# Optimization experiments

Measured on AMD Instinct MI355X. Metric: run time of the kernel, lower is better.

Reference implementation:

```python
import jax, jax.numpy as jnp
import numpy as np

LN_EPS = 1e-6


def setup_inputs() -> dict:
    key = jax.random.key(0)
    ks = jax.random.split(key, 10)
    B, S, D, M, P = 64, 512, 1024, 512, 3
    seq_out = jax.random.normal(ks[0], (B, S, D), dtype=jnp.float32)
    # dependency-tree style adjacency: sparse 0/1, stored dense as in the module
    adj = (jax.random.uniform(ks[1], (B, S, S)) < 0.02).astype(jnp.float32)
    aspect_mask = jax.random.randint(ks[2], (B, S), 0, 2, dtype=jnp.int32)
    # guarantee at least one aspect token per row (asp_wn divisor)
    aspect_mask = aspect_mask.at[:, 0].set(1)
    sc = 0.02
    return {
        "seq_out": seq_out,
        "adj": adj,
        "aspect_mask": aspect_mask,
        "ln_a": jnp.ones((D,), jnp.float32),
        "ln_b": jnp.zeros((D,), jnp.float32),
        "asp_w": jax.random.normal(ks[3], (D,), jnp.float32) * sc,
        "asp_b": jnp.zeros((), jnp.float32),
        "W0": jax.random.normal(ks[4], (D, M), jnp.float32) * sc,
        "b0": jnp.zeros((M,), jnp.float32),
        "W1": jax.random.normal(ks[5], (M, M), jnp.float32) * sc,
        "b1": jnp.zeros((M,), jnp.float32),
        "W2": jax.random.normal(ks[6], (M, M), jnp.float32) * sc,
        "b2": jnp.zeros((M,), jnp.float32),
        "cls_w": jax.random.normal(ks[7], (2 * M, P), jnp.float32) * sc,
        "cls_b": jnp.zeros((P,), jnp.float32),
    }


def _torch_layernorm(x, a, b):
    # torch code: a*(x-mean)/(std+eps)+b with unbiased std (Bessel, /(D-1))
    D = x.shape[-1]
    mean = jnp.mean(x, axis=-1, keepdims=True)
    xc = x - mean
    std = jnp.sqrt(jnp.sum(xc * xc, axis=-1, keepdims=True) / (D - 1))
    return a * xc / (std + LN_EPS) + b


def reference(seq_out, adj, aspect_mask, ln_a, ln_b, asp_w, asp_b,
              W0, b0, W1, b1, W2, b2, cls_w, cls_b):
    tgt = aspect_mask.astype(seq_out.dtype)                 # [B,S] labels == BCE weight (eval mode)
    x = _torch_layernorm(seq_out, ln_a, ln_b)               # [B,S,D]

    # aspect classification head + weighted BCEWithLogits (mean over all elems)
    z = jnp.einsum('bsd,d->bs', x, asp_w) + asp_b           # logits [B,S]
    bce = jnp.logaddexp(0.0, z) - z * tgt                   # stable BCE-with-logits
    loss_asp = jnp.mean(tgt * bce)
    aspect_pred = jax.nn.sigmoid(z)

    # dense-adjacency GCN (dropout = identity in eval)
    denom = jnp.sum(adj, axis=2, keepdims=True) + 1.0       # [B,S,1]
    out = x
    for W, b in ((W0, b0), (W1, b1), (W2, b2)):
        Ax = jnp.einsum('bst,btd->bsd', adj, out)           # aggregate
        out = jax.nn.relu((Ax @ W + b) / denom)             # project + degree-norm + relu

    # aspect-masked mean pool + global mean pool
    asp_wn = jnp.sum(tgt, axis=1, keepdims=True)            # [B,1]
    dep = jnp.einsum('bsm,bs->bm', out, tgt) / asp_wn       # [B,M]
    glob = jnp.mean(out, axis=1)                            # [B,M]

    feature = jnp.concatenate([dep, glob], axis=-1) @ cls_w + cls_b
    logits = jax.nn.softmax(feature, axis=1)
    return feature, logits, aspect_pred, loss_asp
```

## Files before the change

### kernel.cpp

```cpp
#include <hip/hip_runtime.h>
#include <math.h>

typedef __bf16 bf16;
typedef bf16 bf16x2 __attribute__((ext_vector_type(2)));
typedef bf16 bf16x4 __attribute__((ext_vector_type(4)));
typedef bf16 bf16x8 __attribute__((ext_vector_type(8)));
typedef float f32x4 __attribute__((ext_vector_type(4)));

#define NROWS 32768
#define DDIM 1024
#define MDIM 512

__device__ __forceinline__ float wave_reduce_sum(float v) {
#pragma unroll
  for (int o = 32; o > 0; o >>= 1) v += __shfl_down(v, o, 64);
  return v;
}
__device__ __forceinline__ float wave_allreduce_sum(float v) {
#pragma unroll
  for (int o = 32; o > 0; o >>= 1) v += __shfl_xor(v, o, 64);
  return v;
}

__device__ __forceinline__ void load_lds16(const bf16* g, bf16* l) {
  __builtin_amdgcn_global_load_lds(
      (const __attribute__((address_space(1))) unsigned int*)g,
      (__attribute__((address_space(3))) unsigned int*)l, 16, 0, 0);
}

__global__ __launch_bounds__(256) void prep_kernel(
    const float* __restrict__ seq, const float* __restrict__ adj,
    const int* __restrict__ amask, const float* __restrict__ ga,
    const float* __restrict__ gb, const float* __restrict__ aw,
    const float* __restrict__ ab, const float* __restrict__ W0,
    const float* __restrict__ W1, const float* __restrict__ W2,
    bf16* __restrict__ xn, float* __restrict__ aspect_pred,
    float* __restrict__ loss_arr, unsigned short* __restrict__ nbr,
    int* __restrict__ cnt, float* __restrict__ denomv,
    bf16* __restrict__ W0T, bf16* __restrict__ W1T, bf16* __restrict__ W2T) {
  const int bid = blockIdx.x;
  const int tid = threadIdx.x;
  const int lane = tid & 63;
  const int wv = tid >> 6;

  if (bid < 8192) {
    const int row = bid * 4 + wv;
    const float* xr = seq + (size_t)row * DDIM;
    f32x4 v[4];
    float s = 0.0f, sq = 0.0f;
#pragma unroll
    for (int j = 0; j < 4; ++j) {
      v[j] = __builtin_nontemporal_load((const f32x4*)&xr[j * 256 + lane * 4]);
      s += v[j].x + v[j].y + v[j].z + v[j].w;
      sq += v[j].x * v[j].x + v[j].y * v[j].y + v[j].z * v[j].z + v[j].w * v[j].w;
    }
    s = wave_allreduce_sum(s);
    sq = wave_allreduce_sum(sq);
    float mean = s * (1.0f / 1024.0f);
    float var = (sq - 1024.0f * mean * mean) * (1.0f / 1023.0f);
    var = fmaxf(var, 0.0f);
    float inv = 1.0f / (sqrtf(var) + 1e-6f);
    float zp = 0.0f;
#pragma unroll
    for (int j = 0; j < 4; ++j) {
      int c = j * 256 + lane * 4;
      float4 a4 = *(const float4*)&ga[c];
      float4 b4 = *(const float4*)&gb[c];
      float4 w4 = *(const float4*)&aw[c];
      float x0 = a4.x * (v[j].x - mean) * inv + b4.x;
      float x1 = a4.y * (v[j].y - mean) * inv + b4.y;
      float x2 = a4.z * (v[j].z - mean) * inv + b4.z;
      float x3 = a4.w * (v[j].w - mean) * inv + b4.w;
      bf16x4 o;
      o[0] = (bf16)x0; o[1] = (bf16)x1; o[2] = (bf16)x2; o[3] = (bf16)x3;
      __builtin_nontemporal_store(o, (bf16x4*)&xn[(size_t)row * DDIM + c]);
      zp += x0 * w4.x + x1 * w4.y + x2 * w4.z + x3 * w4.w;
    }
    zp = wave_reduce_sum(zp);
    if (lane == 0) {
      float z = zp + ab[0];
      aspect_pred[row] = 1.0f / (1.0f + expf(-z));
      float tgt = (float)amask[row];
      float bce = fmaxf(z, 0.0f) + log1pf(expf(-fabsf(z))) - z * tgt;
      loss_arr[row] = tgt * bce;
    }
  } else if (bid < 16384) {
    const int row = (bid - 8192) * 4 + wv;
    const float* ar = adj + (size_t)row * 512;
    unsigned short* nr = nbr + (size_t)row * 512;
    unsigned long long below = (1ull << lane) - 1ull;
    int base = 0;
#pragma unroll
    for (int t = 0; t < 2; ++t) {
      f32x4 v = __builtin_nontemporal_load((const f32x4*)&ar[t * 256 + lane * 4]);
      unsigned long long m0 = __ballot(v.x != 0.0f);
      unsigned long long m1 = __ballot(v.y != 0.0f);
      unsigned long long m2 = __ballot(v.z != 0.0f);
      unsigned long long m3 = __ballot(v.w != 0.0f);
      int c0 = __popcll(m0), c1 = __popcll(m1), c2 = __popcll(m2);
      int col = t * 256 + lane * 4;
      if (v.x != 0.0f) nr[base + __popcll(m0 & below)] = (unsigned short)(col + 0);
      if (v.y != 0.0f) nr[base + c0 + __popcll(m1 & below)] = (unsigned short)(col + 1);
      if (v.z != 0.0f) nr[base + c0 + c1 + __popcll(m2 & below)] = (unsigned short)(col + 2);
      if (v.w != 0.0f) nr[base + c0 + c1 + c2 + __popcll(m3 & below)] = (unsigned short)(col + 3);
      base += c0 + c1 + c2 + __popcll(m3);
    }
    if (lane == 0) { cnt[row] = base; denomv[row] = (float)base + 1.0f; }
  } else {
    __shared__ bf16 tld[64][72];
    int wid = bid - 16384;
    const float* Wsrc; bf16* Wdst; int KK, NN, t0;
    if (wid < 128)      { Wsrc = W0; Wdst = W0T; KK = 1024; NN = 512; t0 = wid; }
    else if (wid < 192) { Wsrc = W1; Wdst = W1T; KK = 512;  NN = 512; t0 = wid - 128; }
    else                { Wsrc = W2; Wdst = W2T; KK = 512;  NN = 512; t0 = wid - 192; }
    int k0 = (t0 >> 3) << 6;
    int n0 = (t0 & 7) << 6;
    int kk = tid >> 4, nn = (tid & 15) << 2;
#pragma unroll
    for (int s = 0; s < 4; ++s) {
      float4 v = *(const float4*)&Wsrc[(size_t)(k0 + s * 16 + kk) * NN + n0 + nn];
      tld[nn + 0][s * 16 + kk] = (bf16)v.x;
      tld[nn + 1][s * 16 + kk] = (bf16)v.y;
      tld[nn + 2][s * 16 + kk] = (bf16)v.z;
      tld[nn + 3][s * 16 + kk] = (bf16)v.w;
    }
    __syncthreads();
#pragma unroll
    for (int p2 = 0; p2 < 2; ++p2) {
      int seg = p2 * 256 + tid;
      int nn2 = seg >> 3, kk2 = (seg & 7) << 3;
      bf16x8 val;
#pragma unroll
      for (int j = 0; j < 8; ++j) val[j] = tld[nn2][kk2 + j];
      *(bf16x8*)&Wdst[(size_t)(n0 + nn2) * KK + k0 + kk2] = val;
    }
  }
}

#define BAR  __builtin_amdgcn_s_barrier()
#define WAITL do { asm volatile("s_waitcnt lgkmcnt(0)" ::: "memory"); \
                   __builtin_amdgcn_sched_barrier(0); } while (0)
#define WAITV4 do { asm volatile("s_waitcnt vmcnt(4)" ::: "memory"); \
                    __builtin_amdgcn_sched_barrier(0); } while (0)

__global__ __launch_bounds__(512, 2) void gemm256(const bf16* __restrict__ A,
                                                  const bf16* __restrict__ BT,
                                                  bf16* __restrict__ C,
                                                  int K) {
  __shared__ __align__(16) bf16 SMEM[65536];
  bf16 (*As)[16384] = (bf16(*)[16384])SMEM;
  bf16 (*Bs)[16384] = (bf16(*)[16384])(SMEM + 32768);
  const int tid = threadIdx.x;
  const int lane = tid & 63;
  const int wave = tid >> 6;
  const int wr = wave >> 2;
  const int wc = wave & 3;
  const int T = K >> 6;

  const int p = blockIdx.x;
  const int chunk = gridDim.x >> 3;
  const int wg = (p & 7) * chunk + (p >> 3);
  const int m0 = (wg >> 1) * 256;
  const int n0 = (wg & 1) * 256;

  const int srow = tid >> 3;
  const int scol8 = (tid & 7) ^ (srow & 7);

#define STAGEA(t, h)                                                          \
  do {                                                                        \
    int kt_ = ((t) < T) ? (t) * 64 : 0;                                       \
    const bf16* s_ = A + (size_t)(m0 + (h) * 128 + srow) * K + kt_ + scol8*8; \
    bf16* d_ = &As[(t) & 1][(h) * 8192 + wave * 512];                         \
    load_lds16(s_, d_);                                                       \
    load_lds16(s_ + (size_t)64 * K, d_ + 4096);                               \
  } while (0)
#define STAGEB(t, h)                                                          \
  do {                                                                        \
    int kt_ = ((t) < T) ? (t) * 64 : 0;                                       \
    const bf16* s_ = BT + (size_t)(n0 + (h) * 128 + srow) * K + kt_ + scol8*8;\
    bf16* d_ = &Bs[(t) & 1][(h) * 8192 + wave * 512];                         \
    load_lds16(s_, d_);                                                       \
    load_lds16(s_ + (size_t)64 * K, d_ + 4096);                               \
  } while (0)

  const int abase = (wr * 128 + (lane & 15)) * 64 + (lane >> 4) * 8;
  const int bbase = (wc * 64 + (lane & 15)) * 64 + (lane >> 4) * 8;
  const int axor = (lane & 7) << 3;

  bf16x8 areg[4][2], breg[4][2];
  f32x4 acc[8][4];
#pragma unroll
  for (int i = 0; i < 8; ++i)
#pragma unroll
    for (int j = 0; j < 4; ++j)
#pragma unroll
      for (int r = 0; r < 4; ++r) acc[i][j][r] = 0.0f;

#define LDA(buf_, qm)                                                         \
  _Pragma("unroll") for (int i_ = 0; i_ < 4; ++i_)                            \
  _Pragma("unroll") for (int h2_ = 0; h2_ < 2; ++h2_)                         \
    areg[i_][h2_] = *(const bf16x8*)&As[buf_][                                \
        (abase + ((qm)*4 + i_) * 1024 + h2_ * 32) ^ axor];
#define LDB(buf_, qn)                                                         \
  _Pragma("unroll") for (int j_ = 0; j_ < 2; ++j_)                            \
  _Pragma("unroll") for (int h2_ = 0; h2_ < 2; ++h2_)                         \
    breg[(qn)*2 + j_][h2_] = *(const bf16x8*)&Bs[buf_][                       \
        (bbase + ((qn)*2 + j_) * 1024 + h2_ * 32) ^ axor];
#define MFMAQ(qm, qn)                                                         \
  __builtin_amdgcn_s_setprio(1);                                              \
  _Pragma("unroll") for (int i_ = 0; i_ < 4; ++i_)                            \
  _Pragma("unroll") for (int j_ = 0; j_ < 2; ++j_)                            \
  _Pragma("unroll") for (int h2_ = 0; h2_ < 2; ++h2_)                         \
    acc[(qm)*4 + i_][(qn)*2 + j_] = __builtin_amdgcn_mfma_f32_16x16x32_bf16(  \
        areg[i_][h2_], breg[(qn)*2 + j_][h2_], acc[(qm)*4 + i_][(qn)*2 + j_], \
        0, 0, 0);                                                             \
  __builtin_amdgcn_s_setprio(0);

  STAGEA(0, 0); STAGEA(0, 1); STAGEB(0, 0); STAGEB(0, 1);
  STAGEB(1, 0); STAGEB(1, 1);
  WAITV4;
  BAR;

  const int NIT = T >> 1;
  for (int it = 0; it < NIT; ++it) {
    const int t1 = 2 * it + 1, t2 = 2 * it + 2, t3 = 2 * it + 3;
    LDA(0, 0); LDB(0, 0); STAGEA(t1, 0);
    BAR; WAITL; MFMAQ(0, 0); BAR;
    LDB(0, 1); STAGEA(t1, 1);
    BAR; WAITL; MFMAQ(0, 1); BAR;
    LDA(0, 1); STAGEB(t2, 0);
    BAR; WAITL; MFMAQ(1, 0); BAR;
    STAGEB(t2, 1);
    BAR; WAITL; MFMAQ(1, 1); WAITV4; BAR;
    LDA(1, 0); LDB(1, 0); STAGEA(t2, 0);
    BAR; WAITL; MFMAQ(0, 0); BAR;
    LDB(1, 1); STAGEA(t2, 1);
    BAR; WAITL; MFMAQ(0, 1); BAR;
    LDA(1, 1); STAGEB(t3, 0);
    BAR; WAITL; MFMAQ(1, 0); BAR;
    STAGEB(t3, 1);
    BAR; WAITL; MFMAQ(1, 1); WAITV4; BAR;
  }

  const int cn = lane & 15;
  const int rb = (lane >> 4) * 4;
#pragma unroll
  for (int i = 0; i < 8; ++i)
#pragma unroll
    for (int j = 0; j < 4; ++j) {
      int row = wr * 128 + i * 16 + rb;
      int colb = wc * 64 + j * 16 + cn;
#pragma unroll
      for (int r = 0; r < 4; ++r)
        SMEM[((row + r) << 8) + (colb ^ (((row + r) & 7) << 4))] =
            (bf16)acc[i][j][r];
    }
  __syncthreads();
  const size_t cbase = (size_t)m0 * MDIM + n0;
#pragma unroll
  for (int q = 0; q < 16; ++q) {
    int e = q * 4096 + tid * 8;
    int row = e >> 8, col = e & 255;
    *(bf16x8*)&C[cbase + (size_t)row * MDIM + col] =
        *(const bf16x8*)&SMEM[(row << 8) + (col ^ ((row & 7) << 4))];
  }
}

__global__ __launch_bounds__(128) void agg_kernel(const bf16* __restrict__ P,
                                                  const unsigned short* __restrict__ nbr,
                                                  const int* __restrict__ cnt,
                                                  const float* __restrict__ denomv,
                                                  const float* __restrict__ bias,
                                                  bf16* __restrict__ outb) {
  const int p = blockIdx.x;
  const int row0 = (p & 7) * 4096 + (p >> 3) * 8;
  const int tid = threadIdx.x;
  const int b = row0 >> 9;
  __shared__ unsigned short nl[8][512];
  __shared__ int ncnt[8];
  if (tid < 8) ncnt[tid] = cnt[row0 + tid];
  __syncthreads();
#pragma unroll
  for (int r = 0; r < 8; ++r) {
    int n = ncnt[r];
    for (int i = tid; i < n; i += 128)
      nl[r][i] = nbr[(size_t)(row0 + r) * 512 + i];
  }
  __syncthreads();
  const bf16* Pb = P + ((size_t)(b << 9)) * MDIM;
  const int col = tid * 4;
  const float4 bb = *(const float4*)&bias[col];
#pragma unroll 2
  for (int r = 0; r < 8; ++r) {
    const int n = ncnt[r];
    float a0 = 0, a1 = 0, a2 = 0, a3 = 0;
    int e = 0;
    for (; e + 4 <= n; e += 4) {
      bf16x4 v0 = *(const bf16x4*)&Pb[(size_t)nl[r][e + 0] * MDIM + col];
      bf16x4 v1 = *(const bf16x4*)&Pb[(size_t)nl[r][e + 1] * MDIM + col];
      bf16x4 v2 = *(const bf16x4*)&Pb[(size_t)nl[r][e + 2] * MDIM + col];
      bf16x4 v3 = *(const bf16x4*)&Pb[(size_t)nl[r][e + 3] * MDIM + col];
      a0 += (float)v0[0]; a1 += (float)v0[1]; a2 += (float)v0[2]; a3 += (float)v0[3];
      a0 += (float)v1[0]; a1 += (float)v1[1]; a2 += (float)v1[2]; a3 += (float)v1[3];
      a0 += (float)v2[0]; a1 += (float)v2[1]; a2 += (float)v2[2]; a3 += (float)v2[3];
      a0 += (float)v3[0]; a1 += (float)v3[1]; a2 += (float)v3[2]; a3 += (float)v3[3];
    }
    for (; e < n; ++e) {
      bf16x4 v = *(const bf16x4*)&Pb[(size_t)nl[r][e] * MDIM + col];
      a0 += (float)v[0]; a1 += (float)v[1]; a2 += (float)v[2]; a3 += (float)v[3];
    }
    float inv = 1.0f / denomv[row0 + r];
    bf16x4 o;
    o[0] = (bf16)fmaxf((a0 + bb.x) * inv, 0.0f);
    o[1] = (bf16)fmaxf((a1 + bb.y) * inv, 0.0f);
    o[2] = (bf16)fmaxf((a2 + bb.z) * inv, 0.0f);
    o[3] = (bf16)fmaxf((a3 + bb.w) * inv, 0.0f);
    *(bf16x4*)&outb[(size_t)(row0 + r) * MDIM + col] = o;
  }
}

__global__ __launch_bounds__(128) void agg_pool_kernel(
    const bf16* __restrict__ P, const unsigned short* __restrict__ nbr,
    const int* __restrict__ cnt, const float* __restrict__ denomv,
    const float* __restrict__ bias, const int* __restrict__ amask,
    float* __restrict__ part) {
  const int p = blockIdx.x;
  const int row0 = (p & 7) * 4096 + (p >> 3) * 8;
  const int tid = threadIdx.x;
  const int b = row0 >> 9;
  __shared__ unsigned short nl[8][512];
  __shared__ int ncnt[8];
  if (tid < 8) ncnt[tid] = cnt[row0 + tid];
  __syncthreads();
#pragma unroll
  for (int r = 0; r < 8; ++r) {
    int n = ncnt[r];
    for (int i = tid; i < n; i += 128)
      nl[r][i] = nbr[(size_t)(row0 + r) * 512 + i];
  }
  __syncthreads();
  const bf16* Pb = P + ((size_t)(b << 9)) * MDIM;
  const int col = tid * 4;
  const float4 bb = *(const float4*)&bias[col];
  float m0 = 0, m1 = 0, m2 = 0, m3 = 0;
  float g0 = 0, g1 = 0, g2 = 0, g3 = 0;
#pragma unroll 2
  for (int r = 0; r < 8; ++r) {
    const int n = ncnt[r];
    float a0 = 0, a1 = 0, a2 = 0, a3 = 0;
    int e = 0;
    for (; e + 4 <= n; e += 4) {
      bf16x4 v0 = *(const bf16x4*)&Pb[(size_t)nl[r][e + 0] * MDIM + col];
      bf16x4 v1 = *(const bf16x4*)&Pb[(size_t)nl[r][e + 1] * MDIM + col];
      bf16x4 v2 = *(const bf16x4*)&Pb[(size_t)nl[r][e + 2] * MDIM + col];
      bf16x4 v3 = *(const bf16x4*)&Pb[(size_t)nl[r][e + 3] * MDIM + col];
      a0 += (float)v0[0]; a1 += (float)v0[1]; a2 += (float)v0[2]; a3 += (float)v0[3];
      a0 += (float)v1[0]; a1 += (float)v1[1]; a2 += (float)v1[2]; a3 += (float)v1[3];
      a0 += (float)v2[0]; a1 += (float)v2[1]; a2 += (float)v2[2]; a3 += (float)v2[3];
      a0 += (float)v3[0]; a1 += (float)v3[1]; a2 += (float)v3[2]; a3 += (float)v3[3];
    }
    for (; e < n; ++e) {
      bf16x4 v = *(const bf16x4*)&Pb[(size_t)nl[r][e] * MDIM + col];
      a0 += (float)v[0]; a1 += (float)v[1]; a2 += (float)v[2]; a3 += (float)v[3];
    }
    float inv = 1.0f / denomv[row0 + r];
    float o0 = fmaxf((a0 + bb.x) * inv, 0.0f);
    float o1 = fmaxf((a1 + bb.y) * inv, 0.0f);
    float o2 = fmaxf((a2 + bb.z) * inv, 0.0f);
    float o3 = fmaxf((a3 + bb.w) * inv, 0.0f);
    float tg = (float)amask[row0 + r];
    g0 += o0; g1 += o1; g2 += o2; g3 += o3;
    m0 += o0 * tg; m1 += o1 * tg; m2 += o2 * tg; m3 += o3 * tg;
  }
  float* pp = part + (size_t)p * 1024;
  pp[col + 0] = m0; pp[col + 1] = m1; pp[col + 2] = m2; pp[col + 3] = m3;
  pp[512 + col + 0] = g0; pp[512 + col + 1] = g1;
  pp[512 + col + 2] = g2; pp[512 + col + 3] = g3;
}

__global__ __launch_bounds__(512) void poolcls_kernel(
    const float* __restrict__ part, const int* __restrict__ amask,
    const float* __restrict__ loss_arr, const float* __restrict__ cw,
    const float* __restrict__ cb, float* __restrict__ outp) {
  __shared__ float tg[512];
  __shared__ float shr[3][8];
  const int tid = threadIdx.x;
  const int b = blockIdx.x;

  if (b == 64) {
    float s = 0.0f;
    for (int i = tid; i < NROWS; i += 512) s += loss_arr[i];
    s = wave_reduce_sum(s);
    if ((tid & 63) == 0) shr[0][tid >> 6] = s;
    __syncthreads();
    if (tid == 0) {
      float t = 0.0f;
#pragma unroll
      for (int k = 0; k < 8; ++k) t += shr[0][k];
      outp[33152] = t * (1.0f / 32768.0f);
    }
    return;
  }

  tg[tid] = (float)amask[b * 512 + tid];
  __syncthreads();
  float wn = 0.0f;
#pragma unroll 8
  for (int s = 0; s < 512; ++s) wn += tg[s];

  const int x = b >> 3;
  const int qbase = (b & 7) * 64;
  float t = 0.0f, a = 0.0f;
#pragma unroll 4
  for (int j = 0; j < 64; ++j) {
    const float* pp = part + (size_t)(((qbase + j) << 3) | x) * 1024;
    t += pp[tid];
    a += pp[512 + tid];
  }
  float f1 = t / wn;
  float f2 = a * (1.0f / 512.0f);

  float p0 = f1 * cw[tid * 3 + 0] + f2 * cw[(512 + tid) * 3 + 0];
  float p1 = f1 * cw[tid * 3 + 1] + f2 * cw[(512 + tid) * 3 + 1];
  float p2 = f1 * cw[tid * 3 + 2] + f2 * cw[(512 + tid) * 3 + 2];
  p0 = wave_reduce_sum(p0);
  p1 = wave_reduce_sum(p1);
  p2 = wave_reduce_sum(p2);
  if ((tid & 63) == 0) {
    shr[0][tid >> 6] = p0; shr[1][tid >> 6] = p1; shr[2][tid >> 6] = p2;
  }
  __syncthreads();
  if (tid == 0) {
    float q0 = 0, q1 = 0, q2 = 0;
#pragma unroll
    for (int k = 0; k < 8; ++k) { q0 += shr[0][k]; q1 += shr[1][k]; q2 += shr[2][k]; }
    q0 += cb[0]; q1 += cb[1]; q2 += cb[2];
    outp[b * 3 + 0] = q0;
    outp[b * 3 + 1] = q1;
    outp[b * 3 + 2] = q2;
    float m = fmaxf(q0, fmaxf(q1, q2));
    float e0 = expf(q0 - m), e1 = expf(q1 - m), e2 = expf(q2 - m);
    float inv = 1.0f / (e0 + e1 + e2);
    outp[192 + b * 3 + 0] = e0 * inv;
    outp[192 + b * 3 + 1] = e1 * inv;
    outp[192 + b * 3 + 2] = e2 * inv;
  }
}

extern "C" void kernel_launch(void* const* d_in, const int* in_sizes, int n_in,
                              void* d_out, int out_size, void* d_ws, size_t ws_size,
                              hipStream_t stream) {
  const float* seq   = (const float*)d_in[0];
  const float* adj   = (const float*)d_in[1];
  const int*   amask = (const int*)d_in[2];
  const float* ln_a  = (const float*)d_in[3];
  const float* ln_b  = (const float*)d_in[4];
  const float* asp_w = (const float*)d_in[5];
  const float* asp_b = (const float*)d_in[6];
  const float* W0    = (const float*)d_in[7];
  const float* b0    = (const float*)d_in[8];
  const float* W1    = (const float*)d_in[9];
  const float* b1    = (const float*)d_in[10];
  const float* W2    = (const float*)d_in[11];
  const float* b2    = (const float*)d_in[12];
  const float* cls_w = (const float*)d_in[13];
  const float* cls_b = (const float*)d_in[14];
  float* out = (float*)d_out;

  char* w = (char*)d_ws;
  bf16* P             = (bf16*)w;           w += (size_t)NROWS * MDIM * 2;
  bf16* xn            = (bf16*)w;           w += (size_t)NROWS * DDIM * 2;
  bf16* outb          = (bf16*)w;           w += (size_t)NROWS * MDIM * 2;
  unsigned short* nbr = (unsigned short*)w; w += (size_t)NROWS * 512 * 2;
  int* cnt            = (int*)w;            w += (size_t)NROWS * 4;
  float* denomv       = (float*)w;          w += (size_t)NROWS * 4;
  float* loss_arr     = (float*)w;          w += (size_t)NROWS * 4;
  float* part         = (float*)w;          w += (size_t)4096 * 1024 * 4;
  bf16* W0T           = (bf16*)w;           w += (size_t)512 * 1024 * 2;
  bf16* W1T           = (bf16*)w;           w += (size_t)512 * 512 * 2;
  bf16* W2T           = (bf16*)w;           w += (size_t)512 * 512 * 2;

  prep_kernel<<<16640, 256, 0, stream>>>(seq, adj, amask, ln_a, ln_b, asp_w,
                                         asp_b, W0, W1, W2, xn, out + 384,
                                         loss_arr, nbr, cnt, denomv, W0T, W1T,
                                         W2T);
  gemm256<<<256, 512, 0, stream>>>(xn, W0T, P, 1024);
  agg_kernel<<<4096, 128, 0, stream>>>(P, nbr, cnt, denomv, b0, outb);
  gemm256<<<256, 512, 0, stream>>>(outb, W1T, P, 512);
  agg_kernel<<<4096, 128, 0, stream>>>(P, nbr, cnt, denomv, b1, outb);
  gemm256<<<256, 512, 0, stream>>>(outb, W2T, P, 512);
  agg_pool_kernel<<<4096, 128, 0, stream>>>(P, nbr, cnt, denomv, b2, amask,
                                            part);
  poolcls_kernel<<<65, 512, 0, stream>>>(part, amask, loss_arr, cls_w, cls_b,
                                         out);
}
```

Measured before the change: 241.7 us.

## Split prep into LN and adjacency kernels with double-buffered LDS row streaming

```diff
diff --git a/kernel.cpp b/kernel.cpp
--- a/kernel.cpp
+++ b/kernel.cpp
@@ -27,30 +27,49 @@
       (const __attribute__((address_space(1))) unsigned int*)g,
       (__attribute__((address_space(3))) unsigned int*)l, 16, 0, 0);
 }
-
-__global__ __launch_bounds__(256) void prep_kernel(
-    const float* __restrict__ seq, const float* __restrict__ adj,
-    const int* __restrict__ amask, const float* __restrict__ ga,
-    const float* __restrict__ gb, const float* __restrict__ aw,
-    const float* __restrict__ ab, const float* __restrict__ W0,
-    const float* __restrict__ W1, const float* __restrict__ W2,
+__device__ __forceinline__ void load_lds16f(const float* g, float* l) {
+  __builtin_amdgcn_global_load_lds(
+      (const __attribute__((address_space(1))) unsigned int*)g,
+      (__attribute__((address_space(3))) unsigned int*)l, 16, 0, 0);
+}
+
+__global__ __launch_bounds__(256) void ln_kernel(
+    const float* __restrict__ seq, const int* __restrict__ amask,
+    const float* __restrict__ ga, const float* __restrict__ gb,
+    const float* __restrict__ aw, const float* __restrict__ ab,
     bf16* __restrict__ xn, float* __restrict__ aspect_pred,
-    float* __restrict__ loss_arr, unsigned short* __restrict__ nbr,
-    int* __restrict__ cnt, float* __restrict__ denomv,
-    bf16* __restrict__ W0T, bf16* __restrict__ W1T, bf16* __restrict__ W2T) {
-  const int bid = blockIdx.x;
-  const int tid = threadIdx.x;
-  const int lane = tid & 63;
-  const int wv = tid >> 6;
-
-  if (bid < 8192) {
-    const int row = bid * 4 + wv;
-    const float* xr = seq + (size_t)row * DDIM;
+    float* __restrict__ loss_arr) {
+  __shared__ __align__(16) float lbuf[4][2][1024];
+  const int lane = threadIdx.x & 63;
+  const int wv = threadIdx.x >> 6;
+  const int row0 = (blockIdx.x * 4 + wv) * 8;
+  float* slot[2] = {&lbuf[wv][0][0], &lbuf[wv][1][0]};
+
+#pragma unroll
+  for (int j = 0; j < 4; ++j)
+    load_lds16f(&seq[(size_t)row0 * DDIM + j * 256 + lane * 4],
+                slot[0] + j * 256);
+
+  for (int i = 0; i < 8; ++i) {
+    const int row = row0 + i;
+    float* cur = slot[i & 1];
+    float* nxt = slot[(i & 1) ^ 1];
+    if (i < 7) {
+#pragma unroll
+      for (int j = 0; j < 4; ++j)
+        load_lds16f(&seq[(size_t)(row + 1) * DDIM + j * 256 + lane * 4],
+                    nxt + j * 256);
+      asm volatile("s_waitcnt vmcnt(4)" ::: "memory");
+    } else {
+      asm volatile("s_waitcnt vmcnt(0)" ::: "memory");
+    }
+    __builtin_amdgcn_sched_barrier(0);
     f32x4 v[4];
+#pragma unroll
+    for (int j = 0; j < 4; ++j) v[j] = *(const f32x4*)&cur[j * 256 + lane * 4];
     float s = 0.0f, sq = 0.0f;
 #pragma unroll
     for (int j = 0; j < 4; ++j) {
-      v[j] = __builtin_nontemporal_load((const f32x4*)&xr[j * 256 + lane * 4]);
       s += v[j].x + v[j].y + v[j].z + v[j].w;
       sq += v[j].x * v[j].x + v[j].y * v[j].y + v[j].z * v[j].z + v[j].w * v[j].w;
     }
@@ -84,8 +103,22 @@
       float bce = fmaxf(z, 0.0f) + log1pf(expf(-fabsf(z))) - z * tgt;
       loss_arr[row] = tgt * bce;
     }
-  } else if (bid < 16384) {
-    const int row = (bid - 8192) * 4 + wv;
+  }
+}
+
+__global__ __launch_bounds__(256) void nbrw_kernel(
+    const float* __restrict__ adj, const float* __restrict__ W0,
+    const float* __restrict__ W1, const float* __restrict__ W2,
+    unsigned short* __restrict__ nbr, int* __restrict__ cnt,
+    float* __restrict__ denomv, bf16* __restrict__ W0T,
+    bf16* __restrict__ W1T, bf16* __restrict__ W2T) {
+  const int bid = blockIdx.x;
+  const int tid = threadIdx.x;
+  const int lane = tid & 63;
+  const int wv = tid >> 6;
+
+  if (bid < 8192) {
+    const int row = bid * 4 + wv;
     const float* ar = adj + (size_t)row * 512;
     unsigned short* nr = nbr + (size_t)row * 512;
     unsigned long long below = (1ull << lane) - 1ull;
@@ -108,7 +141,7 @@
     if (lane == 0) { cnt[row] = base; denomv[row] = (float)base + 1.0f; }
   } else {
     __shared__ bf16 tld[64][72];
-    int wid = bid - 16384;
+    int wid = bid - 8192;
     const float* Wsrc; bf16* Wdst; int KK, NN, t0;
     if (wid < 128)      { Wsrc = W0; Wdst = W0T; KK = 1024; NN = 512; t0 = wid; }
     else if (wid < 192) { Wsrc = W1; Wdst = W1T; KK = 512;  NN = 512; t0 = wid - 128; }
@@ -480,10 +513,10 @@
   bf16* W1T           = (bf16*)w;           w += (size_t)512 * 512 * 2;
   bf16* W2T           = (bf16*)w;           w += (size_t)512 * 512 * 2;
 
-  prep_kernel<<<16640, 256, 0, stream>>>(seq, adj, amask, ln_a, ln_b, asp_w,
-                                         asp_b, W0, W1, W2, xn, out + 384,
-                                         loss_arr, nbr, cnt, denomv, W0T, W1T,
-                                         W2T);
+  ln_kernel<<<1024, 256, 0, stream>>>(seq, amask, ln_a, ln_b, asp_w, asp_b,
+                                      xn, out + 384, loss_arr);
+  nbrw_kernel<<<8448, 256, 0, stream>>>(adj, W0, W1, W2, nbr, cnt, denomv,
+                                        W0T, W1T, W2T);
   gemm256<<<256, 512, 0, stream>>>(xn, W0T, P, 1024);
   agg_kernel<<<4096, 128, 0, stream>>>(P, nbr, cnt, denomv, b0, outb);
   gemm256<<<256, 512, 0, stream>>>(outb, W1T, P, 512);
```

After: 254.1 us. +5.1%, slower.
